# Kernel tuning notes

Hardware: AMD Instinct MI355X
Metric: run time of the kernel (lower is better)

Reference implementation:

```python
import jax, jax.numpy as jnp
import numpy as np

N_NODES = 100000
N_EDGES = 3200000
N_GRAPHS = 128
IN_DIM = 4
HID = 64
BN_EPS = 1e-5


def setup_inputs() -> dict:
    key = jax.random.key(0)
    ks = jax.random.split(key, 24)
    x = jax.random.normal(ks[0], (N_NODES, IN_DIM), dtype=jnp.float32)
    edge_index = jax.random.randint(ks[1], (2, N_EDGES), 0, N_NODES, dtype=jnp.int32)
    batch_ids = jnp.sort(jax.random.randint(ks[2], (N_NODES,), 0, N_GRAPHS, dtype=jnp.int32))

    def lin(k, out_d, in_d):
        s = 1.0 / np.sqrt(in_d)
        return jax.random.uniform(k, (out_d, in_d), jnp.float32, -s, s)

    inp = {
        'x': x, 'edge_index': edge_index, 'batch_ids': batch_ids,
        # SAGEConv i: out = lin_l(mean_neighbors) + lin_r(x_self); bias lives in lin_l
        'w1l': lin(ks[3], HID, IN_DIM), 'b1': jnp.zeros((HID,), jnp.float32), 'w1r': lin(ks[4], HID, IN_DIM),
        'bn1_g': jnp.ones((HID,), jnp.float32), 'bn1_b': jnp.zeros((HID,), jnp.float32),
        'w2l': lin(ks[5], HID, HID), 'b2': jnp.zeros((HID,), jnp.float32), 'w2r': lin(ks[6], HID, HID),
        'bn2_g': jnp.ones((HID,), jnp.float32), 'bn2_b': jnp.zeros((HID,), jnp.float32),
        'w3l': lin(ks[7], HID, HID), 'b3': jnp.zeros((HID,), jnp.float32), 'w3r': lin(ks[8], HID, HID),
        'bn3_g': jnp.ones((HID,), jnp.float32), 'bn3_b': jnp.zeros((HID,), jnp.float32),
        'fc1_w': lin(ks[9], 64, HID), 'fc1_b': jnp.zeros((64,), jnp.float32),
        'fc2_w': lin(ks[10], 2, 64), 'fc2_b': jnp.zeros((2,), jnp.float32),
    }
    return inp


def _sage(x, src, dst, deg_inv, wl, bl, wr):
    # mean-aggregate neighbor messages (source -> target), then two small GEMMs
    msum = jax.ops.segment_sum(x[src], dst, num_segments=N_NODES)  # [N, d]
    agg = msum * deg_inv[:, None]
    return agg @ wl.T + bl + x @ wr.T


def _bn(x, g, b):
    # BatchNorm1d in training mode: batch stats over node dim, biased variance
    m = jnp.mean(x, axis=0)
    v = jnp.mean((x - m) ** 2, axis=0)
    return (x - m) * jax.lax.rsqrt(v + BN_EPS) * g + b


def reference(x, edge_index, batch_ids,
              w1l, b1, w1r, bn1_g, bn1_b,
              w2l, b2, w2r, bn2_g, bn2_b,
              w3l, b3, w3r, bn3_g, bn3_b,
              fc1_w, fc1_b, fc2_w, fc2_b):
    src, dst = edge_index[0], edge_index[1]
    deg = jax.ops.segment_sum(jnp.ones((src.shape[0],), x.dtype), dst, num_segments=N_NODES)
    deg_inv = 1.0 / jnp.maximum(deg, 1.0)

    h = jax.nn.relu(_bn(_sage(x, src, dst, deg_inv, w1l, b1, w1r), bn1_g, bn1_b))
    h = jax.nn.relu(_bn(_sage(h, src, dst, deg_inv, w2l, b2, w2r), bn2_g, bn2_b))
    h = jax.nn.relu(_bn(_sage(h, src, dst, deg_inv, w3l, b3, w3r), bn3_g, bn3_b))

    # global_mean_pool over graphs
    gsum = jax.ops.segment_sum(h, batch_ids, num_segments=N_GRAPHS)
    gcnt = jax.ops.segment_sum(jnp.ones((h.shape[0],), h.dtype), batch_ids, num_segments=N_GRAPHS)
    pooled = gsum / jnp.maximum(gcnt, 1.0)[:, None]

    # MLP head (dropout = identity at inference)
    hid = jax.nn.relu(pooled @ fc1_w.T + fc1_b)
    return hid @ fc2_w.T + fc2_b
```

## Files before the change

### kernel.cpp

```cpp
#include <hip/hip_runtime.h>
#include <hip/hip_fp16.h>

#define NN 100000
#define NE 3200000
#define NG 128
#define BN_EPS 1e-5f

#define NBUK 782
#define BSHIFT 7
#define BCAP 6144

#define GRID_SG 1024
#define PBMAX 2048

typedef _Float16 h2v __attribute__((ext_vector_type(2)));


__global__ void __launch_bounds__(512) k_scatter(
    const int* __restrict__ src, const int* __restrict__ dst,
    int* __restrict__ slab_cursor, unsigned int* __restrict__ slab, int E) {
    __shared__ int hist[NBUK + 2];
    __shared__ int cbase[NBUK + 2];
    int tid = threadIdx.x;
    int eBeg = blockIdx.x * 6250;
    int eEnd = min(eBeg + 6250, E);

    for (int t = tid; t < NBUK; t += 512) hist[t] = 0;
    __syncthreads();
    for (int e = eBeg + tid; e < eEnd; e += 512) {
        int b = dst[e] >> BSHIFT;
        atomicAdd(&hist[b], 1);
    }
    __syncthreads();
    for (int t = tid; t < NBUK; t += 512) {
        int c = hist[t];
        cbase[t] = (c > 0) ? atomicAdd(&slab_cursor[t], c) : 0;
    }
    __syncthreads();
    for (int t = tid; t < NBUK; t += 512) hist[t] = 0;
    __syncthreads();
    for (int e = eBeg + tid; e < eEnd; e += 512) {
        int d = dst[e];
        int b = d >> BSHIFT;
        int r = atomicAdd(&hist[b], 1);
        int pos = cbase[b] + r;
        if (pos < BCAP) slab[(size_t)b * BCAP + pos] = ((unsigned)src[e] << BSHIFT) | (unsigned)(d & 127);
    }
}

__global__ void k_bucket_scan(const int* __restrict__ slab_cursor,
                              int* __restrict__ bucket_base, int* __restrict__ row_ptr) {
    __shared__ int sm[1024];
    int t = threadIdx.x;
    int c = (t < NBUK) ? min(slab_cursor[t], BCAP) : 0;
    sm[t] = c;
    __syncthreads();
    for (int off = 1; off < 1024; off <<= 1) {
        int add = (t >= off) ? sm[t - off] : 0;
        __syncthreads();
        sm[t] += add;
        __syncthreads();
    }
    if (t < NBUK) {
        bucket_base[t] = sm[t] - c;
        if (t == NBUK - 1) row_ptr[NN] = sm[t];
    }
}

__global__ void __launch_bounds__(512) k_bucket_csr(
    const unsigned int* __restrict__ slab, const int* __restrict__ slab_cursor,
    const int* __restrict__ bucket_base, int* __restrict__ row_ptr,
    float* __restrict__ deg_inv, int* __restrict__ csr_src,
    const float* __restrict__ x, const float* __restrict__ w1l,
    const float* __restrict__ b1, const float* __restrict__ w1r,
    float* __restrict__ h_pre, float* __restrict__ part) {
    __shared__ int lds_csr[BCAP];
    __shared__ int sdeg[128];
    __shared__ int sscan[128];
    __shared__ int slcur[128];
    __shared__ float swl[256], swr[256], sb1[64];
    __shared__ float ssum[64], ssq[64];
    int tid = threadIdx.x;
    int b = blockIdx.x;
    int lo = b << BSHIFT;
    int cnt = min(slab_cursor[b], BCAP);
    const unsigned int* sl = slab + (size_t)b * BCAP;

    if (tid < 256) { swl[tid] = w1l[tid]; swr[tid] = w1r[tid]; }
    if (tid < 64)  { sb1[tid] = b1[tid]; ssum[tid] = 0.f; ssq[tid] = 0.f; }
    if (tid < 128) sdeg[tid] = 0;
    __syncthreads();
    for (int k = tid; k < cnt; k += 512) {
        atomicAdd(&sdeg[sl[k] & 127], 1);
    }
    __syncthreads();
    int v = (tid < 128) ? sdeg[tid] : 0;
    if (tid < 128) sscan[tid] = v;
    __syncthreads();
    for (int off = 1; off < 128; off <<= 1) {
        int add = 0;
        if (tid < 128 && tid >= off) add = sscan[tid - off];
        __syncthreads();
        if (tid < 128) sscan[tid] += add;
        __syncthreads();
    }
    int base = bucket_base[b];
    if (tid < 128) {
        int excl = sscan[tid] - v;
        int n = lo + tid;
        if (n < NN) {
            row_ptr[n] = base + excl;
            deg_inv[n] = 1.0f / fmaxf((float)v, 1.0f);
        }
        slcur[tid] = excl;
    }
    __syncthreads();
    for (int k = tid; k < cnt; k += 512) {
        unsigned int p = sl[k];
        int pos = atomicAdd(&slcur[p & 127], 1);
        lds_csr[pos] = (int)(p >> BSHIFT);
    }
    __syncthreads();
    for (int k = tid; k < cnt; k += 512) csr_src[base + k] = lds_csr[k];

    int i = tid >> 2, c = tid & 3;
    int n = lo + i;
    bool valid = (n < NN);
    int dhi = sscan[i];
    int dlo = dhi - sdeg[i];
    const float4* x4 = (const float4*)x;
    float4 acc = make_float4(0.f, 0.f, 0.f, 0.f);
    for (int k = dlo + c; k < dhi; k += 4) {
        int s = lds_csr[k];
        float4 xv = x4[s];
        acc.x += xv.x; acc.y += xv.y; acc.z += xv.z; acc.w += xv.w;
    }
#pragma unroll
    for (int m = 1; m <= 2; m <<= 1) {
        acc.x += __shfl_xor(acc.x, m);
        acc.y += __shfl_xor(acc.y, m);
        acc.z += __shfl_xor(acc.z, m);
        acc.w += __shfl_xor(acc.w, m);
    }
    float dv = 1.0f / fmaxf((float)sdeg[i], 1.0f);
    float ax = acc.x * dv, ay = acc.y * dv, az = acc.z * dv, aw = acc.w * dv;
    float4 xs = valid ? x4[n] : make_float4(0.f, 0.f, 0.f, 0.f);

#pragma unroll
    for (int m4 = 0; m4 < 4; m4++) {
        float4 o = make_float4(0.f, 0.f, 0.f, 0.f);
        float* op = &o.x;
        if (valid) {
#pragma unroll
            for (int t = 0; t < 4; t++) {
                int j = c * 16 + m4 * 4 + t;
                float s = sb1[j];
                s += ax * swl[j * 4 + 0] + ay * swl[j * 4 + 1] + az * swl[j * 4 + 2] + aw * swl[j * 4 + 3];
                s += xs.x * swr[j * 4 + 0] + xs.y * swr[j * 4 + 1] + xs.z * swr[j * 4 + 2] + xs.w * swr[j * 4 + 3];
                op[t] = s;
            }
            ((float4*)h_pre)[(size_t)n * 16 + c * 4 + m4] = o;
        }
        float4 q = make_float4(o.x * o.x, o.y * o.y, o.z * o.z, o.w * o.w);
#pragma unroll
        for (int m = 4; m <= 32; m <<= 1) {
            o.x += __shfl_xor(o.x, m); o.y += __shfl_xor(o.y, m);
            o.z += __shfl_xor(o.z, m); o.w += __shfl_xor(o.w, m);
            q.x += __shfl_xor(q.x, m); q.y += __shfl_xor(q.y, m);
            q.z += __shfl_xor(q.z, m); q.w += __shfl_xor(q.w, m);
        }
        if ((tid & 63) < 4) {
            int jb = c * 16 + m4 * 4;
            atomicAdd(&ssum[jb + 0], o.x); atomicAdd(&ssum[jb + 1], o.y);
            atomicAdd(&ssum[jb + 2], o.z); atomicAdd(&ssum[jb + 3], o.w);
            atomicAdd(&ssq[jb + 0], q.x);  atomicAdd(&ssq[jb + 1], q.y);
            atomicAdd(&ssq[jb + 2], q.z);  atomicAdd(&ssq[jb + 3], q.w);
        }
    }
    __syncthreads();
    if (tid < 64) {
        part[(2 * tid) * PBMAX + blockIdx.x]     = ssum[tid];
        part[(2 * tid + 1) * PBMAX + blockIdx.x] = ssq[tid];
    }
}

__global__ void __launch_bounds__(512, 8) k_sage(
    const __half* __restrict__ h_in, const int* __restrict__ row_ptr,
    const int* __restrict__ csr_src, const float* __restrict__ deg_inv,
    const float* __restrict__ wl, const float* __restrict__ bl,
    const float* __restrict__ wr, float* __restrict__ h_pre,
    float* __restrict__ part) {
    __shared__ h2v wl2s[32][68];
    __shared__ h2v wr2s[32][68];
    __shared__ h2v tAh[32][36];
    __shared__ h2v tXh[32][36];
    __shared__ float ssum[64], ssq[64];
    int tid = threadIdx.x;
    for (int idx = tid; idx < 2048; idx += 512) {
        int j = idx & 63, kk = idx >> 6;
        float2 l = ((const float2*)wl)[j * 32 + kk];
        float2 r = ((const float2*)wr)[j * 32 + kk];
        wl2s[kk][j] = h2v{(_Float16)l.x, (_Float16)l.y};
        wr2s[kk][j] = h2v{(_Float16)r.x, (_Float16)r.y};
    }
    if (tid < 64) { ssum[tid] = 0.f; ssq[tid] = 0.f; }
    __syncthreads();

    int g = tid & 15, ni = tid >> 4;
    const uint2* tbl = (const uint2*)h_in;
    const int ntiles = NN / 32;

    for (int tile = blockIdx.x; tile < ntiles; tile += GRID_SG) {
        int n = tile * 32 + ni;
        float ax = 0.f, ay = 0.f, az = 0.f, aw = 0.f;
        int r0 = row_ptr[n], r1 = row_ptr[n + 1];
        int e = r0;
        for (; e + 8 <= r1; e += 8) {
            int s0 = csr_src[e],     s1 = csr_src[e + 1], s2 = csr_src[e + 2], s3 = csr_src[e + 3];
            int s4 = csr_src[e + 4], s5 = csr_src[e + 5], s6 = csr_src[e + 6], s7 = csr_src[e + 7];
            uint2 v0 = tbl[(size_t)s0 * 16 + g];
            uint2 v1 = tbl[(size_t)s1 * 16 + g];
            uint2 v2 = tbl[(size_t)s2 * 16 + g];
            uint2 v3 = tbl[(size_t)s3 * 16 + g];
            uint2 v4 = tbl[(size_t)s4 * 16 + g];
            uint2 v5 = tbl[(size_t)s5 * 16 + g];
            uint2 v6 = tbl[(size_t)s6 * 16 + g];
            uint2 v7 = tbl[(size_t)s7 * 16 + g];
            float2 f;
            f = __half22float2(*(__half2*)&v0.x); ax += f.x; ay += f.y;
            f = __half22float2(*(__half2*)&v0.y); az += f.x; aw += f.y;
            f = __half22float2(*(__half2*)&v1.x); ax += f.x; ay += f.y;
            f = __half22float2(*(__half2*)&v1.y); az += f.x; aw += f.y;
            f = __half22float2(*(__half2*)&v2.x); ax += f.x; ay += f.y;
            f = __half22float2(*(__half2*)&v2.y); az += f.x; aw += f.y;
            f = __half22float2(*(__half2*)&v3.x); ax += f.x; ay += f.y;
            f = __half22float2(*(__half2*)&v3.y); az += f.x; aw += f.y;
            f = __half22float2(*(__half2*)&v4.x); ax += f.x; ay += f.y;
            f = __half22float2(*(__half2*)&v4.y); az += f.x; aw += f.y;
            f = __half22float2(*(__half2*)&v5.x); ax += f.x; ay += f.y;
            f = __half22float2(*(__half2*)&v5.y); az += f.x; aw += f.y;
            f = __half22float2(*(__half2*)&v6.x); ax += f.x; ay += f.y;
            f = __half22float2(*(__half2*)&v6.y); az += f.x; aw += f.y;
            f = __half22float2(*(__half2*)&v7.x); ax += f.x; ay += f.y;
            f = __half22float2(*(__half2*)&v7.y); az += f.x; aw += f.y;
        }
        for (; e < r1; ++e) {
            int s = csr_src[e];
            uint2 v = tbl[(size_t)s * 16 + g];
            float2 f;
            f = __half22float2(*(__half2*)&v.x); ax += f.x; ay += f.y;
            f = __half22float2(*(__half2*)&v.y); az += f.x; aw += f.y;
        }
        float di = deg_inv[n];
        uint2 rsv = tbl[(size_t)n * 16 + g];
        ax *= di; ay *= di; az *= di; aw *= di;
        tAh[ni][2 * g]     = h2v{(_Float16)ax, (_Float16)ay};
        tAh[ni][2 * g + 1] = h2v{(_Float16)az, (_Float16)aw};
        *(uint2*)&tXh[ni][2 * g] = rsv;
        __syncthreads();

        float4 o = ((const float4*)bl)[g];
#pragma unroll 4
        for (int kk = 0; kk < 32; kk++) {
            h2v a2 = tAh[ni][kk];
            h2v x2 = tXh[ni][kk];
            h2v l0 = wl2s[kk][4 * g + 0], l1 = wl2s[kk][4 * g + 1];
            h2v l2 = wl2s[kk][4 * g + 2], l3 = wl2s[kk][4 * g + 3];
            h2v r0v = wr2s[kk][4 * g + 0], r1v = wr2s[kk][4 * g + 1];
            h2v r2v = wr2s[kk][4 * g + 2], r3v = wr2s[kk][4 * g + 3];
#if __has_builtin(__builtin_amdgcn_fdot2)
            o.x = __builtin_amdgcn_fdot2(a2, l0, o.x, false);
            o.y = __builtin_amdgcn_fdot2(a2, l1, o.y, false);
            o.z = __builtin_amdgcn_fdot2(a2, l2, o.z, false);
            o.w = __builtin_amdgcn_fdot2(a2, l3, o.w, false);
            o.x = __builtin_amdgcn_fdot2(x2, r0v, o.x, false);
            o.y = __builtin_amdgcn_fdot2(x2, r1v, o.y, false);
            o.z = __builtin_amdgcn_fdot2(x2, r2v, o.z, false);
            o.w = __builtin_amdgcn_fdot2(x2, r3v, o.w, false);
#else
            float b0 = (float)a2.x, b1 = (float)a2.y, x0 = (float)x2.x, x1 = (float)x2.y;
            o.x += b0 * (float)l0.x + b1 * (float)l0.y + x0 * (float)r0v.x + x1 * (float)r0v.y;
            o.y += b0 * (float)l1.x + b1 * (float)l1.y + x0 * (float)r1v.x + x1 * (float)r1v.y;
            o.z += b0 * (float)l2.x + b1 * (float)l2.y + x0 * (float)r2v.x + x1 * (float)r2v.y;
            o.w += b0 * (float)l3.x + b1 * (float)l3.y + x0 * (float)r3v.x + x1 * (float)r3v.y;
#endif
        }
        ((float4*)h_pre)[(size_t)n * 16 + g] = o;

        float4 qv = make_float4(o.x * o.x, o.y * o.y, o.z * o.z, o.w * o.w);
#pragma unroll
        for (int m = 16; m <= 32; m <<= 1) {
            o.x += __shfl_xor(o.x, m); o.y += __shfl_xor(o.y, m);
            o.z += __shfl_xor(o.z, m); o.w += __shfl_xor(o.w, m);
            qv.x += __shfl_xor(qv.x, m); qv.y += __shfl_xor(qv.y, m);
            qv.z += __shfl_xor(qv.z, m); qv.w += __shfl_xor(qv.w, m);
        }
        if ((tid & 48) == 0) {
            atomicAdd(&ssum[4 * g + 0], o.x); atomicAdd(&ssum[4 * g + 1], o.y);
            atomicAdd(&ssum[4 * g + 2], o.z); atomicAdd(&ssum[4 * g + 3], o.w);
            atomicAdd(&ssq[4 * g + 0], qv.x);  atomicAdd(&ssq[4 * g + 1], qv.y);
            atomicAdd(&ssq[4 * g + 2], qv.z);  atomicAdd(&ssq[4 * g + 3], qv.w);
        }
        __syncthreads();
    }
    if (tid < 64) {
        part[(2 * tid) * PBMAX + blockIdx.x]     = ssum[tid];
        part[(2 * tid + 1) * PBMAX + blockIdx.x] = ssq[tid];
    }
}

__global__ void k_reduce_sb(const float* __restrict__ part, int PB,
                            const float* __restrict__ gamma, const float* __restrict__ beta,
                            float* __restrict__ sbv, int N) {
    int c = blockIdx.x;
    float s = 0.f, q = 0.f;
    for (int b = threadIdx.x; b < PB; b += 256) {
        s += part[(2 * c) * PBMAX + b];
        q += part[(2 * c + 1) * PBMAX + b];
    }
    __shared__ float rs[256], rq[256];
    rs[threadIdx.x] = s;
    rq[threadIdx.x] = q;
    __syncthreads();
    for (int off = 128; off > 0; off >>= 1) {
        if (threadIdx.x < off) {
            rs[threadIdx.x] += rs[threadIdx.x + off];
            rq[threadIdx.x] += rq[threadIdx.x + off];
        }
        __syncthreads();
    }
    if (threadIdx.x == 0) {
        float m = rs[0] / (float)N;
        float var = rq[0] / (float)N - m * m;
        float sc = gamma[c] * rsqrtf(var + BN_EPS);
        sbv[c]      = sc;
        sbv[64 + c] = beta[c] - m * sc;
    }
}

__global__ void k_bnrelu_h(const float* __restrict__ h_pre, const float* __restrict__ sbv,
                           __half* __restrict__ h, int N) {
    __shared__ float s_sc[64], s_bi[64];
    if (threadIdx.x < 64) {
        s_sc[threadIdx.x] = sbv[threadIdx.x];
        s_bi[threadIdx.x] = sbv[64 + threadIdx.x];
    }
    __syncthreads();
    int total = N * 16;
    for (int i = blockIdx.x * blockDim.x + threadIdx.x; i < total; i += gridDim.x * blockDim.x) {
        float4 v = ((const float4*)h_pre)[i];
        int c4 = (i & 15) * 4;
        v.x = fmaxf(v.x * s_sc[c4 + 0] + s_bi[c4 + 0], 0.f);
        v.y = fmaxf(v.y * s_sc[c4 + 1] + s_bi[c4 + 1], 0.f);
        v.z = fmaxf(v.z * s_sc[c4 + 2] + s_bi[c4 + 2], 0.f);
        v.w = fmaxf(v.w * s_sc[c4 + 3] + s_bi[c4 + 3], 0.f);
        __half2 p0 = __floats2half2_rn(v.x, v.y);
        __half2 p1 = __floats2half2_rn(v.z, v.w);
        uint2 o;
        o.x = *(unsigned int*)&p0;
        o.y = *(unsigned int*)&p1;
        ((uint2*)h)[i] = o;
    }
}

__global__ void k_poolhead(const float* __restrict__ hB, const float* __restrict__ sbv,
                           const int* __restrict__ batch,
                           const float* __restrict__ fc1w, const float* __restrict__ fc1b,
                           const float* __restrict__ fc2w, const float* __restrict__ fc2b,
                           float* __restrict__ out, int N) {
    __shared__ float ssc[64], sbi[64];
    __shared__ float sm[256];
    __shared__ float pl[64], hid[64];
    if (threadIdx.x < 64) {
        ssc[threadIdx.x] = sbv[threadIdx.x];
        sbi[threadIdx.x] = sbv[64 + threadIdx.x];
    }
    __syncthreads();
    int gph = blockIdx.x;
    int lo = 0, hi = N;
    while (lo < hi) { int mid = (lo + hi) >> 1; if (batch[mid] < gph) lo = mid + 1; else hi = mid; }
    int start = lo;
    hi = N;
    while (lo < hi) { int mid = (lo + hi) >> 1; if (batch[mid] < gph + 1) lo = mid + 1; else hi = mid; }
    int end = lo;

    int c = threadIdx.x & 63, w = threadIdx.x >> 6;
    float s = 0.f;
    for (int r = start + w; r < end; r += 4)
        s += fmaxf(hB[(size_t)r * 64 + c] * ssc[c] + sbi[c], 0.f);
    sm[threadIdx.x] = s;
    __syncthreads();
    if (threadIdx.x < 64) {
        float t = sm[c] + sm[64 + c] + sm[128 + c] + sm[192 + c];
        pl[c] = t / fmaxf((float)(end - start), 1.0f);
    }
    __syncthreads();
    if (threadIdx.x < 64) {
        int j = threadIdx.x;
        float v = fc1b[j];
        for (int k = 0; k < 64; k++) v += pl[k] * fc1w[j * 64 + k];
        hid[j] = fmaxf(v, 0.f);
    }
    __syncthreads();
    if (threadIdx.x < 2) {
        int j = threadIdx.x;
        float o = fc2b[j];
        for (int k = 0; k < 64; k++) o += hid[k] * fc2w[j * 64 + k];
        out[gph * 2 + j] = o;
    }
}

extern "C" void kernel_launch(void* const* d_in, const int* in_sizes, int n_in,
                              void* d_out, int out_size, void* d_ws, size_t ws_size,
                              hipStream_t stream) {
    const float* x    = (const float*)d_in[0];
    const int* ei     = (const int*)d_in[1];
    const int* batch  = (const int*)d_in[2];
    const float* w1l  = (const float*)d_in[3];
    const float* b1   = (const float*)d_in[4];
    const float* w1r  = (const float*)d_in[5];
    const float* bn1g = (const float*)d_in[6];
    const float* bn1b = (const float*)d_in[7];
    const float* w2l  = (const float*)d_in[8];
    const float* b2   = (const float*)d_in[9];
    const float* w2r  = (const float*)d_in[10];
    const float* bn2g = (const float*)d_in[11];
    const float* bn2b = (const float*)d_in[12];
    const float* w3l  = (const float*)d_in[13];
    const float* b3   = (const float*)d_in[14];
    const float* w3r  = (const float*)d_in[15];
    const float* bn3g = (const float*)d_in[16];
    const float* bn3b = (const float*)d_in[17];
    const float* fc1w = (const float*)d_in[18];
    const float* fc1b = (const float*)d_in[19];
    const float* fc2w = (const float*)d_in[20];
    const float* fc2b = (const float*)d_in[21];
    float* out = (float*)d_out;

    const int N = NN, E = NE;
    const int* srcp = ei;
    const int* dstp = ei + E;

    char* ws = (char*)d_ws;
    size_t off = 0;
    auto alloc = [&](size_t bytes) -> char* {
        char* p = ws + off;
        off += (bytes + 255) & ~(size_t)255;
        return p;
    };
    int* csr_src       = (int*)alloc(sizeof(int) * E);
    float* hB          = (float*)alloc(sizeof(float) * N * 64);
    __half* hH         = (__half*)alloc(sizeof(__half) * N * 64);
    unsigned int* slab = (unsigned int*)alloc(sizeof(unsigned int) * (size_t)NBUK * BCAP);
    int* slab_cursor   = (int*)alloc(sizeof(int) * NBUK);
    int* bucket_base   = (int*)alloc(sizeof(int) * NBUK);
    int* row_ptr       = (int*)alloc(sizeof(int) * (N + 1));
    float* deg_inv     = (float*)alloc(sizeof(float) * N);
    float* part        = (float*)alloc(sizeof(float) * 128 * PBMAX);
    float* sbv         = (float*)alloc(sizeof(float) * 128);

    hipMemsetAsync(slab_cursor, 0, sizeof(int) * NBUK, stream);

    k_scatter<<<512, 512, 0, stream>>>(srcp, dstp, slab_cursor, slab, E);
    k_bucket_scan<<<1, 1024, 0, stream>>>(slab_cursor, bucket_base, row_ptr);
    k_bucket_csr<<<NBUK, 512, 0, stream>>>(slab, slab_cursor, bucket_base, row_ptr, deg_inv,
                                           csr_src, x, w1l, b1, w1r, hB, part);
    k_reduce_sb<<<64, 256, 0, stream>>>(part, NBUK, bn1g, bn1b, sbv, N);
    k_bnrelu_h<<<1024, 256, 0, stream>>>(hB, sbv, hH, N);

    k_sage<<<GRID_SG, 512, 0, stream>>>(hH, row_ptr, csr_src, deg_inv, w2l, b2, w2r, hB, part);
    k_reduce_sb<<<64, 256, 0, stream>>>(part, GRID_SG, bn2g, bn2b, sbv, N);
    k_bnrelu_h<<<1024, 256, 0, stream>>>(hB, sbv, hH, N);

    k_sage<<<GRID_SG, 512, 0, stream>>>(hH, row_ptr, csr_src, deg_inv, w3l, b3, w3r, hB, part);
    k_reduce_sb<<<64, 256, 0, stream>>>(part, GRID_SG, bn3g, bn3b, sbv, N);
    k_poolhead<<<NG, 256, 0, stream>>>(hB, sbv, batch, fc1w, fc1b, fc2w, fc2b, out, N);
}
```

Measured before the change: 446.8 us.

## Store pre-BN activations in fp16, fold bucket scan into CSR kernel, add nontemporal hints

Pre-BatchNorm activations are now written and read as fp16 instead of fp32, which halves the traffic of the intermediate buffer across the sage, bnrelu and poolhead kernels. The separate single-block bucket scan kernel is removed. Each CSR block now computes its own base offset by reducing the slab cursors of all earlier buckets, which saves a launch but repeats that reduction work in every block. Nontemporal load and store hints are added to streaming accesses of the slab, csr_src and the activation buffers. Rounding to fp16 before the BN statistics are applied adds some precision loss.

Measured after the change: 558.7 us. +25.1%, slower.

```diff
diff --git a/kernel.cpp b/kernel.cpp
--- a/kernel.cpp
+++ b/kernel.cpp
@@ -14,6 +14,8 @@
 #define PBMAX 2048
 
 typedef _Float16 h2v __attribute__((ext_vector_type(2)));
+typedef unsigned int u32x2 __attribute__((ext_vector_type(2)));
+typedef unsigned int u32x4 __attribute__((ext_vector_type(4)));
 
 
 __global__ void __launch_bounds__(512) k_scatter(
@@ -44,37 +46,22 @@
         int b = d >> BSHIFT;
         int r = atomicAdd(&hist[b], 1);
         int pos = cbase[b] + r;
-        if (pos < BCAP) slab[(size_t)b * BCAP + pos] = ((unsigned)src[e] << BSHIFT) | (unsigned)(d & 127);
-    }
-}
-
-__global__ void k_bucket_scan(const int* __restrict__ slab_cursor,
-                              int* __restrict__ bucket_base, int* __restrict__ row_ptr) {
-    __shared__ int sm[1024];
-    int t = threadIdx.x;
-    int c = (t < NBUK) ? min(slab_cursor[t], BCAP) : 0;
-    sm[t] = c;
-    __syncthreads();
-    for (int off = 1; off < 1024; off <<= 1) {
-        int add = (t >= off) ? sm[t - off] : 0;
-        __syncthreads();
-        sm[t] += add;
-        __syncthreads();
-    }
-    if (t < NBUK) {
-        bucket_base[t] = sm[t] - c;
-        if (t == NBUK - 1) row_ptr[NN] = sm[t];
+        int s = __builtin_nontemporal_load(&src[e]);
+        if (pos < BCAP)
+            __builtin_nontemporal_store(((unsigned)s << BSHIFT) | (unsigned)(d & 127),
+                                        &slab[(size_t)b * BCAP + pos]);
     }
 }
 
 __global__ void __launch_bounds__(512) k_bucket_csr(
     const unsigned int* __restrict__ slab, const int* __restrict__ slab_cursor,
-    const int* __restrict__ bucket_base, int* __restrict__ row_ptr,
+    int* __restrict__ row_ptr,
     float* __restrict__ deg_inv, int* __restrict__ csr_src,
     const float* __restrict__ x, const float* __restrict__ w1l,
     const float* __restrict__ b1, const float* __restrict__ w1r,
-    float* __restrict__ h_pre, float* __restrict__ part) {
+    __half* __restrict__ hp16, float* __restrict__ part) {
     __shared__ int lds_csr[BCAP];
+    __shared__ int red[512];
     __shared__ int sdeg[128];
     __shared__ int sscan[128];
     __shared__ int slcur[128];
@@ -86,6 +73,17 @@
     int cnt = min(slab_cursor[b], BCAP);
     const unsigned int* sl = slab + (size_t)b * BCAP;
 
+    int partial = 0;
+    for (int j = tid; j < b; j += 512) partial += min(slab_cursor[j], BCAP);
+    red[tid] = partial;
+    __syncthreads();
+    for (int off = 256; off > 0; off >>= 1) {
+        if (tid < off) red[tid] += red[tid + off];
+        __syncthreads();
+    }
+    int base = red[0];
+    if (b == NBUK - 1 && tid == 0) row_ptr[NN] = base + cnt;
+
     if (tid < 256) { swl[tid] = w1l[tid]; swr[tid] = w1r[tid]; }
     if (tid < 64)  { sb1[tid] = b1[tid]; ssum[tid] = 0.f; ssq[tid] = 0.f; }
     if (tid < 128) sdeg[tid] = 0;
@@ -104,7 +102,6 @@
         if (tid < 128) sscan[tid] += add;
         __syncthreads();
     }
-    int base = bucket_base[b];
     if (tid < 128) {
         int excl = sscan[tid] - v;
         int n = lo + tid;
@@ -121,7 +118,8 @@
         lds_csr[pos] = (int)(p >> BSHIFT);
     }
     __syncthreads();
-    for (int k = tid; k < cnt; k += 512) csr_src[base + k] = lds_csr[k];
+    for (int k = tid; k < cnt; k += 512)
+        __builtin_nontemporal_store(lds_csr[k], &csr_src[base + k]);
 
     int i = tid >> 2, c = tid & 3;
     int n = lo + i;
@@ -159,7 +157,12 @@
                 s += xs.x * swr[j * 4 + 0] + xs.y * swr[j * 4 + 1] + xs.z * swr[j * 4 + 2] + xs.w * swr[j * 4 + 3];
                 op[t] = s;
             }
-            ((float4*)h_pre)[(size_t)n * 16 + c * 4 + m4] = o;
+            h2v p0 = h2v{(_Float16)o.x, (_Float16)o.y};
+            h2v p1 = h2v{(_Float16)o.z, (_Float16)o.w};
+            u32x2 w;
+            w.x = *(unsigned int*)&p0;
+            w.y = *(unsigned int*)&p1;
+            __builtin_nontemporal_store(w, (u32x2*)hp16 + (size_t)n * 16 + c * 4 + m4);
         }
         float4 q = make_float4(o.x * o.x, o.y * o.y, o.z * o.z, o.w * o.w);
 #pragma unroll
@@ -188,7 +191,7 @@
     const __half* __restrict__ h_in, const int* __restrict__ row_ptr,
     const int* __restrict__ csr_src, const float* __restrict__ deg_inv,
     const float* __restrict__ wl, const float* __restrict__ bl,
-    const float* __restrict__ wr, float* __restrict__ h_pre,
+    const float* __restrict__ wr, __half* __restrict__ hp16,
     float* __restrict__ part) {
     __shared__ h2v wl2s[32][68];
     __shared__ h2v wr2s[32][68];
@@ -216,8 +219,14 @@
         int r0 = row_ptr[n], r1 = row_ptr[n + 1];
         int e = r0;
         for (; e + 8 <= r1; e += 8) {
-            int s0 = csr_src[e],     s1 = csr_src[e + 1], s2 = csr_src[e + 2], s3 = csr_src[e + 3];
-            int s4 = csr_src[e + 4], s5 = csr_src[e + 5], s6 = csr_src[e + 6], s7 = csr_src[e + 7];
+            int s0 = __builtin_nontemporal_load(&csr_src[e]);
+            int s1 = __builtin_nontemporal_load(&csr_src[e + 1]);
+            int s2 = __builtin_nontemporal_load(&csr_src[e + 2]);
+            int s3 = __builtin_nontemporal_load(&csr_src[e + 3]);
+            int s4 = __builtin_nontemporal_load(&csr_src[e + 4]);
+            int s5 = __builtin_nontemporal_load(&csr_src[e + 5]);
+            int s6 = __builtin_nontemporal_load(&csr_src[e + 6]);
+            int s7 = __builtin_nontemporal_load(&csr_src[e + 7]);
             uint2 v0 = tbl[(size_t)s0 * 16 + g];
             uint2 v1 = tbl[(size_t)s1 * 16 + g];
             uint2 v2 = tbl[(size_t)s2 * 16 + g];
@@ -245,7 +254,7 @@
             f = __half22float2(*(__half2*)&v7.y); az += f.x; aw += f.y;
         }
         for (; e < r1; ++e) {
-            int s = csr_src[e];
+            int s = __builtin_nontemporal_load(&csr_src[e]);
             uint2 v = tbl[(size_t)s * 16 + g];
             float2 f;
             f = __half22float2(*(__half2*)&v.x); ax += f.x; ay += f.y;
@@ -285,7 +294,14 @@
             o.w += b0 * (float)l3.x + b1 * (float)l3.y + x0 * (float)r3v.x + x1 * (float)r3v.y;
 #endif
         }
-        ((float4*)h_pre)[(size_t)n * 16 + g] = o;
+        {
+            h2v p0 = h2v{(_Float16)o.x, (_Float16)o.y};
+            h2v p1 = h2v{(_Float16)o.z, (_Float16)o.w};
+            u32x2 w;
+            w.x = *(unsigned int*)&p0;
+            w.y = *(unsigned int*)&p1;
+            __builtin_nontemporal_store(w, (u32x2*)hp16 + (size_t)n * 16 + g);
+        }
 
         float4 qv = make_float4(o.x * o.x, o.y * o.y, o.z * o.z, o.w * o.w);
 #pragma unroll
@@ -338,7 +354,7 @@
     }
 }
 
-__global__ void k_bnrelu_h(const float* __restrict__ h_pre, const float* __restrict__ sbv,
+__global__ void k_bnrelu_h(const __half* __restrict__ hp16, const float* __restrict__ sbv,
                            __half* __restrict__ h, int N) {
     __shared__ float s_sc[64], s_bi[64];
     if (threadIdx.x < 64) {
@@ -346,24 +362,26 @@
         s_bi[threadIdx.x] = sbv[64 + threadIdx.x];
     }
     __syncthreads();
-    int total = N * 16;
+    int total = N * 8;
     for (int i = blockIdx.x * blockDim.x + threadIdx.x; i < total; i += gridDim.x * blockDim.x) {
-        float4 v = ((const float4*)h_pre)[i];
-        int c4 = (i & 15) * 4;
-        v.x = fmaxf(v.x * s_sc[c4 + 0] + s_bi[c4 + 0], 0.f);
-        v.y = fmaxf(v.y * s_sc[c4 + 1] + s_bi[c4 + 1], 0.f);
-        v.z = fmaxf(v.z * s_sc[c4 + 2] + s_bi[c4 + 2], 0.f);
-        v.w = fmaxf(v.w * s_sc[c4 + 3] + s_bi[c4 + 3], 0.f);
-        __half2 p0 = __floats2half2_rn(v.x, v.y);
-        __half2 p1 = __floats2half2_rn(v.z, v.w);
-        uint2 o;
-        o.x = *(unsigned int*)&p0;
-        o.y = *(unsigned int*)&p1;
-        ((uint2*)h)[i] = o;
-    }
-}
-
-__global__ void k_poolhead(const float* __restrict__ hB, const float* __restrict__ sbv,
+        u32x4 raw = __builtin_nontemporal_load((const u32x4*)hp16 + i);
+        int c8 = (i & 7) * 8;
+        u32x4 outw;
+#pragma unroll
+        for (int p = 0; p < 4; p++) {
+            unsigned int rw = raw[p];
+            float2 f = __half22float2(*(__half2*)&rw);
+            int cc = c8 + p * 2;
+            f.x = fmaxf(f.x * s_sc[cc + 0] + s_bi[cc + 0], 0.f);
+            f.y = fmaxf(f.y * s_sc[cc + 1] + s_bi[cc + 1], 0.f);
+            __half2 pk = __floats2half2_rn(f.x, f.y);
+            outw[p] = *(unsigned int*)&pk;
+        }
+        ((u32x4*)h)[i] = outw;
+    }
+}
+
+__global__ void k_poolhead(const __half* __restrict__ hp16, const float* __restrict__ sbv,
                            const int* __restrict__ batch,
                            const float* __restrict__ fc1w, const float* __restrict__ fc1b,
                            const float* __restrict__ fc2w, const float* __restrict__ fc2b,
@@ -387,7 +405,7 @@
     int c = threadIdx.x & 63, w = threadIdx.x >> 6;
     float s = 0.f;
     for (int r = start + w; r < end; r += 4)
-        s += fmaxf(hB[(size_t)r * 64 + c] * ssc[c] + sbi[c], 0.f);
+        s += fmaxf(__half2float(hp16[(size_t)r * 64 + c]) * ssc[c] + sbi[c], 0.f);
     sm[threadIdx.x] = s;
     __syncthreads();
     if (threadIdx.x < 64) {
@@ -449,11 +467,10 @@
         return p;
     };
     int* csr_src       = (int*)alloc(sizeof(int) * E);
-    float* hB          = (float*)alloc(sizeof(float) * N * 64);
+    __half* hp16       = (__half*)alloc(sizeof(__half) * N * 64);
     __half* hH         = (__half*)alloc(sizeof(__half) * N * 64);
     unsigned int* slab = (unsigned int*)alloc(sizeof(unsigned int) * (size_t)NBUK * BCAP);
     int* slab_cursor   = (int*)alloc(sizeof(int) * NBUK);
-    int* bucket_base   = (int*)alloc(sizeof(int) * NBUK);
     int* row_ptr       = (int*)alloc(sizeof(int) * (N + 1));
     float* deg_inv     = (float*)alloc(sizeof(float) * N);
     float* part        = (float*)alloc(sizeof(float) * 128 * PBMAX);
@@ -462,17 +479,16 @@
     hipMemsetAsync(slab_cursor, 0, sizeof(int) * NBUK, stream);
 
     k_scatter<<<512, 512, 0, stream>>>(srcp, dstp, slab_cursor, slab, E);
-    k_bucket_scan<<<1, 1024, 0, stream>>>(slab_cursor, bucket_base, row_ptr);
-    k_bucket_csr<<<NBUK, 512, 0, stream>>>(slab, slab_cursor, bucket_base, row_ptr, deg_inv,
-                                           csr_src, x, w1l, b1, w1r, hB, part);
+    k_bucket_csr<<<NBUK, 512, 0, stream>>>(slab, slab_cursor, row_ptr, deg_inv,
+                                           csr_src, x, w1l, b1, w1r, hp16, part);
     k_reduce_sb<<<64, 256, 0, stream>>>(part, NBUK, bn1g, bn1b, sbv, N);
-    k_bnrelu_h<<<1024, 256, 0, stream>>>(hB, sbv, hH, N);
-
-    k_sage<<<GRID_SG, 512, 0, stream>>>(hH, row_ptr, csr_src, deg_inv, w2l, b2, w2r, hB, part);
+    k_bnrelu_h<<<1024, 256, 0, stream>>>(hp16, sbv, hH, N);
+
+    k_sage<<<GRID_SG, 512, 0, stream>>>(hH, row_ptr, csr_src, deg_inv, w2l, b2, w2r, hp16, part);
     k_reduce_sb<<<64, 256, 0, stream>>>(part, GRID_SG, bn2g, bn2b, sbv, N);
-    k_bnrelu_h<<<1024, 256, 0, stream>>>(hB, sbv, hH, N);
-
-    k_sage<<<GRID_SG, 512, 0, stream>>>(hH, row_ptr, csr_src, deg_inv, w3l, b3, w3r, hB, part);
+    k_bnrelu_h<<<1024, 256, 0, stream>>>(hp16, sbv, hH, N);
+
+    k_sage<<<GRID_SG, 512, 0, stream>>>(hH, row_ptr, csr_src, deg_inv, w3l, b3, w3r, hp16, part);
     k_reduce_sb<<<64, 256, 0, stream>>>(part, GRID_SG, bn3g, bn3b, sbv, N);
-    k_poolhead<<<NG, 256, 0, stream>>>(hB, sbv, batch, fc1w, fc1b, fc2w, fc2b, out, N);
-}
+    k_poolhead<<<NG, 256, 0, stream>>>(hp16, sbv, batch, fc1w, fc1b, fc2w, fc2b, out, N);
+}
```
